# Kernel optimization log

Hardware: AMD Instinct MI355X
Metric: run time of the kernel (lower is better)

## Reference

```python
import jax, jax.numpy as jnp
import numpy as np


def setup_inputs() -> dict:
    key = jax.random.key(0)
    kq, kv, ks = jax.random.split(key, 3)
    B, T, nh, N, D = 4, 2048, 8, 64, 128
    Q = jax.random.normal(kq, (B, T, nh, N), dtype=jnp.float32)
    V = jax.random.normal(kv, (B, T, D), dtype=jnp.float32)
    state = jax.random.normal(ks, (B, nh, N, D), dtype=jnp.float32)
    return {"Q": Q, "V": V, "state": state, "return_new_state": 1}


def reference(Q, V, state, return_new_state):
    # Inter-chunk: read recurrent state.  Q:[B,T,nh,N] x state:[B,nh,N,D] -> [B,T,nh,D]
    output = jnp.einsum('BTnN,BnND->BTnD', Q, state)
    new_state = None
    if return_new_state:
        # Q.flatten(2).mT @ V, unflattened: outer-product accumulation Q^T V
        new_state = state + jnp.einsum('BTnN,BTD->BnND', Q, V)
    T = Q.shape[1]
    if T > 1:
        # Strictly-causal intra-chunk term: tril(QQ^T, -1) @ V
        scores = jnp.tril(jnp.einsum('BTnN,BUnN->BnTU', Q, Q), k=-1)
        output = output + jnp.einsum('BnTU,BUD->BTnD', scores, V)
    return (output, new_state)
```

## Files before the change

kernel.cpp:

```cpp
#include <hip/hip_runtime.h>


using floatx4 = __attribute__((ext_vector_type(4))) float;
using float4v = __attribute__((ext_vector_type(4))) float;
using float2v = __attribute__((ext_vector_type(2))) float;
using shortx8 = __attribute__((ext_vector_type(8))) short;
using shortx4 = __attribute__((ext_vector_type(4))) short;
using uint2v  = __attribute__((ext_vector_type(2))) unsigned int;

#define MFMA16(a, b, c) __builtin_amdgcn_mfma_f32_16x16x32_bf16((a), (b), (c), 0, 0, 0)

__device__ __forceinline__ unsigned short f2bf(float f) {
  unsigned int u = __builtin_bit_cast(unsigned int, f);
  u += 0x7FFFu + ((u >> 16) & 1u);
  return (unsigned short)(u >> 16);
}
__device__ __forceinline__ float bf2f(unsigned short h) {
  unsigned int u = ((unsigned int)h) << 16;
  return __builtin_bit_cast(float, u);
}
__device__ __forceinline__ unsigned int pack2(float a, float b) {
  return (unsigned int)f2bf(a) | ((unsigned int)f2bf(b) << 16);
}
__device__ __forceinline__ shortx8 lds8(const unsigned short* p) {
  shortx4 a = *(const shortx4*)p;
  shortx4 b = *(const shortx4*)(p + 4);
  return __builtin_shufflevector(a, b, 0, 1, 2, 3, 4, 5, 6, 7);
}

#define DECODE_BNC()                                    \
  const int id = blockIdx.x;                            \
  const int n = (id >> 3) & 7;                          \
  const int bc = (id >> 6) * 8 + (id & 7);              \
  const int b = bc >> 5, c = bc & 31

__global__ __launch_bounds__(256) void k_phase1(const float* __restrict__ Q,
                                                const float* __restrict__ V,
                                                unsigned short* __restrict__ ws1) {
  __shared__ unsigned short Qt[64 * 68];
  __shared__ unsigned short Vt[128 * 68];

  DECODE_BNC();
  const int tid = threadIdx.x;
  const float* qbase = Q + (((size_t)(b * 2048 + c * 64) * 8 + n) * 64);
  const float* vbase = V + ((size_t)(b * 2048 + c * 64) * 128);

#pragma unroll
  for (int it = 0; it < 8; ++it) {
    int j = tid + it * 256;
    int i = j & 63, p = j >> 6;
    float q0 = qbase[(2 * p) * 512 + i];
    float q1 = qbase[(2 * p + 1) * 512 + i];
    *(unsigned int*)&Qt[i * 68 + 2 * p] = pack2(q0, q1);
  }
#pragma unroll
  for (int it = 0; it < 16; ++it) {
    int j = tid + it * 256;
    int d = j & 127, p = j >> 7;
    float v0 = vbase[(2 * p) * 128 + d];
    float v1 = vbase[(2 * p + 1) * 128 + d];
    *(unsigned int*)&Vt[d * 68 + 2 * p] = pack2(v0, v1);
  }
  __syncthreads();

  const int wave = tid >> 6, lane = tid & 63;
  const int col = lane & 15, quad = lane >> 4;

  floatx4 acc[4][2];
#pragma unroll
  for (int ti = 0; ti < 4; ++ti)
#pragma unroll
    for (int dj = 0; dj < 2; ++dj) acc[ti][dj] = (floatx4){0.f, 0.f, 0.f, 0.f};

#pragma unroll
  for (int s = 0; s < 2; ++s) {
    const int koff = s * 32 + quad * 8;
    shortx8 bv[2];
#pragma unroll
    for (int dj = 0; dj < 2; ++dj)
      bv[dj] = lds8(&Vt[((wave * 2 + dj) * 16 + col) * 68 + koff]);
#pragma unroll
    for (int ti = 0; ti < 4; ++ti) {
      shortx8 aq = lds8(&Qt[(ti * 16 + col) * 68 + koff]);
#pragma unroll
      for (int dj = 0; dj < 2; ++dj) acc[ti][dj] = MFMA16(aq, bv[dj], acc[ti][dj]);
    }
  }

  unsigned short* wbase = ws1 + (size_t)((b * 8 + n) * 32 + c) * 8192;
#pragma unroll
  for (int ti = 0; ti < 4; ++ti)
#pragma unroll
    for (int dj = 0; dj < 2; ++dj)
#pragma unroll
      for (int r = 0; r < 4; ++r) {
        int i = ti * 16 + quad * 4 + r;
        int d = (wave * 2 + dj) * 16 + col;
        wbase[i * 128 + d] = f2bf(acc[ti][dj][r]);
      }
}

__global__ __launch_bounds__(256) void k_prefix(const float* __restrict__ state,
                                                const unsigned int* __restrict__ ws1,
                                                unsigned int* __restrict__ ws2,
                                                float* __restrict__ new_state) {
  int t = blockIdx.x * 256 + threadIdx.x;
  int bn = t >> 12;
  int e2 = t & 4095;
  float2v st = *(const float2v*)(state + (size_t)bn * 8192 + 2 * e2);
  float run0 = st.x, run1 = st.y;
  const unsigned int* w1 = ws1 + (size_t)bn * 32 * 4096 + e2;
  unsigned int* w2 = ws2 + (size_t)bn * 32 * 4096 + e2;
#pragma unroll
  for (int g = 0; g < 32; ++g) {
    w2[g * 4096] = pack2(run0, run1);
    unsigned int s = w1[g * 4096];
    run0 += bf2f((unsigned short)(s & 0xFFFFu));
    run1 += bf2f((unsigned short)(s >> 16));
  }
  float2v ns; ns.x = run0; ns.y = run1;
  *(float2v*)(new_state + (size_t)bn * 8192 + 2 * e2) = ns;
}

__global__ __launch_bounds__(256) void k_phase2(const float* __restrict__ Q,
                                                const float* __restrict__ V,
                                                const unsigned short* __restrict__ ws2,
                                                float* __restrict__ out) {
  __shared__ unsigned short Qs[64 * 72];
  __shared__ unsigned short Vt[128 * 68];
  __shared__ unsigned short Ss[64 * 72];
  __shared__ unsigned short Pt[128 * 68];

  DECODE_BNC();
  const int tid = threadIdx.x;
  const int wave = tid >> 6, lane = tid & 63;
  const int col = lane & 15, quad = lane >> 4;

  {
    const unsigned int* pb32 =
        (const unsigned int*)(ws2 + (size_t)((b * 8 + n) * 32 + c) * 8192);
#pragma unroll
    for (int it = 0; it < 16; ++it) {
      int j = tid + it * 256;
      int d2 = j & 63, i = j >> 6;
      unsigned int u = pb32[i * 64 + d2];
      Pt[(2 * d2) * 68 + i] = (unsigned short)(u & 0xFFFFu);
      Pt[(2 * d2 + 1) * 68 + i] = (unsigned short)(u >> 16);
    }
  }

  const float* qbase = Q + (((size_t)(b * 2048 + c * 64) * 8 + n) * 64);
  const float* vbase = V + ((size_t)(b * 2048 + c * 64) * 128);
  float* obase = out + (((size_t)(b * 2048 + c * 64) * 8 + n) * 128);

#pragma unroll
  for (int it = 0; it < 4; ++it) {
    int l = tid + it * 256;
    int t = l >> 4, k4 = (l & 15) * 4;
    float4v q = *(const float4v*)(qbase + (size_t)t * 512 + k4);
    uint2v u;
    u.x = pack2(q.x, q.y);
    u.y = pack2(q.z, q.w);
    *(uint2v*)&Qs[t * 72 + k4] = u;
  }
#pragma unroll
  for (int it = 0; it < 16; ++it) {
    int j = tid + it * 256;
    int d = j & 127, p = j >> 7;
    float v0 = vbase[(size_t)(2 * p) * 128 + d];
    float v1 = vbase[(size_t)(2 * p + 1) * 128 + d];
    *(unsigned int*)&Vt[d * 68 + 2 * p] = pack2(v0, v1);
  }
  __syncthreads();

  {
    int job = 0;
    for (int ti = 0; ti < 4; ++ti)
      for (int ui = 0; ui <= (ti | 1); ++ui, ++job) {
        if ((job & 3) != wave) continue;
        if (ui > ti) {
#pragma unroll
          for (int r = 0; r < 4; ++r)
            Ss[(ti * 16 + quad * 4 + r) * 72 + ui * 16 + col] = 0;
        } else {
          floatx4 sc = (floatx4){0.f, 0.f, 0.f, 0.f};
#pragma unroll
          for (int s = 0; s < 2; ++s) {
            shortx8 at = *(const shortx8*)&Qs[(ti * 16 + col) * 72 + s * 32 + quad * 8];
            shortx8 au = *(const shortx8*)&Qs[(ui * 16 + col) * 72 + s * 32 + quad * 8];
            sc = MFMA16(at, au, sc);
          }
#pragma unroll
          for (int r = 0; r < 4; ++r) {
            int t = ti * 16 + quad * 4 + r, u = ui * 16 + col;
            Ss[t * 72 + u] = (u < t) ? f2bf(sc[r]) : (unsigned short)0;
          }
        }
      }
  }
  __syncthreads();

  floatx4 acc[4][2];
#pragma unroll
  for (int ti = 0; ti < 4; ++ti)
#pragma unroll
    for (int dj = 0; dj < 2; ++dj) acc[ti][dj] = (floatx4){0.f, 0.f, 0.f, 0.f};

#pragma unroll
  for (int s = 0; s < 2; ++s) {
    const int koff = s * 32 + quad * 8;
    shortx8 bp[2];
#pragma unroll
    for (int dj = 0; dj < 2; ++dj)
      bp[dj] = lds8(&Pt[((wave * 2 + dj) * 16 + col) * 68 + koff]);
#pragma unroll
    for (int ti = 0; ti < 4; ++ti) {
      shortx8 aq = *(const shortx8*)&Qs[(ti * 16 + col) * 72 + koff];
#pragma unroll
      for (int dj = 0; dj < 2; ++dj) acc[ti][dj] = MFMA16(aq, bp[dj], acc[ti][dj]);
    }
  }
#pragma unroll
  for (int s = 0; s < 2; ++s) {
    const int koff = s * 32 + quad * 8;
    shortx8 bv[2];
#pragma unroll
    for (int dj = 0; dj < 2; ++dj)
      bv[dj] = lds8(&Vt[((wave * 2 + dj) * 16 + col) * 68 + koff]);
    for (int ti = (s == 0 ? 0 : 2); ti < 4; ++ti) {
      shortx8 as = *(const shortx8*)&Ss[(ti * 16 + col) * 72 + koff];
#pragma unroll
      for (int dj = 0; dj < 2; ++dj) acc[ti][dj] = MFMA16(as, bv[dj], acc[ti][dj]);
    }
  }
#pragma unroll
  for (int ti = 0; ti < 4; ++ti)
#pragma unroll
    for (int dj = 0; dj < 2; ++dj)
#pragma unroll
      for (int r = 0; r < 4; ++r) {
        int t = ti * 16 + quad * 4 + r;
        int d = (wave * 2 + dj) * 16 + col;
        obase[(size_t)t * 1024 + d] = acc[ti][dj][r];
      }
}

extern "C" void kernel_launch(void* const* d_in, const int* in_sizes, int n_in,
                              void* d_out, int out_size, void* d_ws, size_t ws_size,
                              hipStream_t stream) {
  (void)in_sizes; (void)n_in; (void)out_size; (void)ws_size;
  const float* Q     = (const float*)d_in[0];
  const float* V     = (const float*)d_in[1];
  const float* state = (const float*)d_in[2];
  float* out        = (float*)d_out;
  float* new_state  = out + (size_t)4 * 2048 * 8 * 128;
  unsigned short* ws1 = (unsigned short*)d_ws;
  unsigned short* ws2 = ws1 + (size_t)32 * 32 * 8192;

  k_phase1<<<1024, 256, 0, stream>>>(Q, V, ws1);
  k_prefix<<<512, 256, 0, stream>>>(state, (const unsigned int*)ws1,
                                    (unsigned int*)ws2, new_state);
  k_phase2<<<1024, 256, 0, stream>>>(Q, V, ws2, out);
}
```

Baseline: 104.6 us.

## Fuse three phases into one cooperative kernel with grid-wide syncs

Replaces the three separate launches (phase1, prefix scan, phase2) with one cooperative kernel of 512 blocks that runs each phase back to back, separated by grid.sync barriers. Each block handles two chunk jobs per phase, and the original three launches remain as a fallback if the cooperative launch fails. The goal is to remove launch gaps and inter-kernel drain. In exchange, occupancy is capped at two blocks per CU, work per block is serialized, and grid barriers add cost. The bf16 pack helper also switches to the library conversion intrinsic.

After: 345.0 us. 230% more time.

```diff
diff --git a/kernel.cpp b/kernel.cpp
--- a/kernel.cpp
+++ b/kernel.cpp
@@ -1,4 +1,8 @@
 #include <hip/hip_runtime.h>
+#include <hip/hip_bf16.h>
+#include <hip/hip_cooperative_groups.h>
+
+namespace cg = cooperative_groups;
 
 
 using floatx4 = __attribute__((ext_vector_type(4))) float;
@@ -20,7 +24,10 @@
   return __builtin_bit_cast(float, u);
 }
 __device__ __forceinline__ unsigned int pack2(float a, float b) {
-  return (unsigned int)f2bf(a) | ((unsigned int)f2bf(b) << 16);
+  __hip_bfloat162 h = __float22bfloat162_rn(float2{a, b});
+  unsigned int u;
+  __builtin_memcpy(&u, &h, 4);
+  return u;
 }
 __device__ __forceinline__ shortx8 lds8(const unsigned short* p) {
   shortx4 a = *(const shortx4*)p;
@@ -28,20 +35,20 @@
   return __builtin_shufflevector(a, b, 0, 1, 2, 3, 4, 5, 6, 7);
 }
 
-#define DECODE_BNC()                                    \
-  const int id = blockIdx.x;                            \
-  const int n = (id >> 3) & 7;                          \
-  const int bc = (id >> 6) * 8 + (id & 7);              \
+#define DECODE_JOB(job)                                 \
+  const int n = ((job) >> 3) & 7;                       \
+  const int bc = ((job) >> 6) * 8 + ((job) & 7);        \
   const int b = bc >> 5, c = bc & 31
 
-__global__ __launch_bounds__(256) void k_phase1(const float* __restrict__ Q,
-                                                const float* __restrict__ V,
-                                                unsigned short* __restrict__ ws1) {
-  __shared__ unsigned short Qt[64 * 68];
-  __shared__ unsigned short Vt[128 * 68];
-
-  DECODE_BNC();
-  const int tid = threadIdx.x;
+__device__ __forceinline__ void phase1_body(int job, int tid,
+                                            const float* __restrict__ Q,
+                                            const float* __restrict__ V,
+                                            unsigned short* __restrict__ ws1,
+                                            unsigned short* Qt,
+                                            unsigned short* Vt) {
+  DECODE_JOB(job);
+  const int wave = tid >> 6, lane = tid & 63;
+  const int col = lane & 15, quad = lane >> 4;
   const float* qbase = Q + (((size_t)(b * 2048 + c * 64) * 8 + n) * 64);
   const float* vbase = V + ((size_t)(b * 2048 + c * 64) * 128);
 
@@ -63,9 +70,6 @@
   }
   __syncthreads();
 
-  const int wave = tid >> 6, lane = tid & 63;
-  const int col = lane & 15, quad = lane >> 4;
-
   floatx4 acc[4][2];
 #pragma unroll
   for (int ti = 0; ti < 4; ++ti)
@@ -100,17 +104,17 @@
       }
 }
 
-__global__ __launch_bounds__(256) void k_prefix(const float* __restrict__ state,
-                                                const unsigned int* __restrict__ ws1,
-                                                unsigned int* __restrict__ ws2,
-                                                float* __restrict__ new_state) {
-  int t = blockIdx.x * 256 + threadIdx.x;
+__device__ __forceinline__ void prefix_body(int t,
+                                            const float* __restrict__ state,
+                                            const unsigned int* __restrict__ w1base,
+                                            unsigned int* __restrict__ w2base,
+                                            float* __restrict__ new_state) {
   int bn = t >> 12;
   int e2 = t & 4095;
   float2v st = *(const float2v*)(state + (size_t)bn * 8192 + 2 * e2);
   float run0 = st.x, run1 = st.y;
-  const unsigned int* w1 = ws1 + (size_t)bn * 32 * 4096 + e2;
-  unsigned int* w2 = ws2 + (size_t)bn * 32 * 4096 + e2;
+  const unsigned int* w1 = w1base + (size_t)bn * 131072 + e2;
+  unsigned int* w2 = w2base + (size_t)bn * 131072 + e2;
 #pragma unroll
   for (int g = 0; g < 32; ++g) {
     w2[g * 4096] = pack2(run0, run1);
@@ -122,17 +126,16 @@
   *(float2v*)(new_state + (size_t)bn * 8192 + 2 * e2) = ns;
 }
 
-__global__ __launch_bounds__(256) void k_phase2(const float* __restrict__ Q,
-                                                const float* __restrict__ V,
-                                                const unsigned short* __restrict__ ws2,
-                                                float* __restrict__ out) {
-  __shared__ unsigned short Qs[64 * 72];
-  __shared__ unsigned short Vt[128 * 68];
-  __shared__ unsigned short Ss[64 * 72];
-  __shared__ unsigned short Pt[128 * 68];
-
-  DECODE_BNC();
-  const int tid = threadIdx.x;
+__device__ __forceinline__ void phase2_body(int job, int tid,
+                                            const float* __restrict__ Q,
+                                            const float* __restrict__ V,
+                                            const unsigned short* __restrict__ ws2,
+                                            float* __restrict__ out,
+                                            unsigned short* Qs,
+                                            unsigned short* Vt,
+                                            unsigned short* Ss,
+                                            unsigned short* Pt) {
+  DECODE_JOB(job);
   const int wave = tid >> 6, lane = tid & 63;
   const int col = lane & 15, quad = lane >> 4;
 
@@ -148,7 +151,6 @@
       Pt[(2 * d2 + 1) * 68 + i] = (unsigned short)(u >> 16);
     }
   }
-
   const float* qbase = Q + (((size_t)(b * 2048 + c * 64) * 8 + n) * 64);
   const float* vbase = V + ((size_t)(b * 2048 + c * 64) * 128);
   float* obase = out + (((size_t)(b * 2048 + c * 64) * 8 + n) * 128);
@@ -174,10 +176,10 @@
   __syncthreads();
 
   {
-    int job = 0;
+    int w = 0;
     for (int ti = 0; ti < 4; ++ti)
-      for (int ui = 0; ui <= (ti | 1); ++ui, ++job) {
-        if ((job & 3) != wave) continue;
+      for (int ui = 0; ui <= (ti | 1); ++ui, ++w) {
+        if ((w & 3) != wave) continue;
         if (ui > ti) {
 #pragma unroll
           for (int r = 0; r < 4; ++r)
@@ -243,6 +245,60 @@
         int d = (wave * 2 + dj) * 16 + col;
         obase[(size_t)t * 1024 + d] = acc[ti][dj][r];
       }
+}
+
+__global__ __launch_bounds__(256, 2) void k_fused(
+    const float* __restrict__ Q, const float* __restrict__ V,
+    const float* __restrict__ state, unsigned short* __restrict__ ws1,
+    unsigned short* __restrict__ ws2, float* __restrict__ out,
+    float* __restrict__ new_state) {
+  __shared__ __align__(16) unsigned short smem[26624];
+  cg::grid_group grid = cg::this_grid();
+
+  const int bid = blockIdx.x;
+  const int tid = threadIdx.x;
+
+  phase1_body(bid, tid, Q, V, ws1, smem, smem + 4352);
+  __syncthreads();
+  phase1_body(bid + 512, tid, Q, V, ws1, smem, smem + 4352);
+
+  __threadfence();
+  grid.sync();
+
+  prefix_body(bid * 256 + tid, state, (const unsigned int*)ws1,
+              (unsigned int*)ws2, new_state);
+
+  __threadfence();
+  grid.sync();
+
+  phase2_body(bid, tid, Q, V, ws2, out,
+              smem, smem + 4608, smem + 13312, smem + 17920);
+  __syncthreads();
+  phase2_body(bid + 512, tid, Q, V, ws2, out,
+              smem, smem + 4608, smem + 13312, smem + 17920);
+}
+
+__global__ __launch_bounds__(256) void k_phase1(const float* __restrict__ Q,
+                                                const float* __restrict__ V,
+                                                unsigned short* __restrict__ ws1) {
+  __shared__ __align__(16) unsigned short smem[13056];
+  phase1_body(blockIdx.x, threadIdx.x, Q, V, ws1, smem, smem + 4352);
+}
+
+__global__ __launch_bounds__(256) void k_prefix(const float* __restrict__ state,
+                                                const unsigned int* __restrict__ ws1,
+                                                unsigned int* __restrict__ ws2,
+                                                float* __restrict__ new_state) {
+  prefix_body(blockIdx.x * 256 + threadIdx.x, state, ws1, ws2, new_state);
+}
+
+__global__ __launch_bounds__(256) void k_phase2(const float* __restrict__ Q,
+                                                const float* __restrict__ V,
+                                                const unsigned short* __restrict__ ws2,
+                                                float* __restrict__ out) {
+  __shared__ __align__(16) unsigned short smem[26624];
+  phase2_body(blockIdx.x, threadIdx.x, Q, V, ws2, out,
+              smem, smem + 4608, smem + 13312, smem + 17920);
 }
 
 extern "C" void kernel_launch(void* const* d_in, const int* in_sizes, int n_in,
@@ -257,8 +313,14 @@
   unsigned short* ws1 = (unsigned short*)d_ws;
   unsigned short* ws2 = ws1 + (size_t)32 * 32 * 8192;
 
-  k_phase1<<<1024, 256, 0, stream>>>(Q, V, ws1);
-  k_prefix<<<512, 256, 0, stream>>>(state, (const unsigned int*)ws1,
-                                    (unsigned int*)ws2, new_state);
-  k_phase2<<<1024, 256, 0, stream>>>(Q, V, ws2, out);
-}
+  void* args[] = {(void*)&Q, (void*)&V, (void*)&state, (void*)&ws1,
+                  (void*)&ws2, (void*)&out, (void*)&new_state};
+  hipError_t err = hipLaunchCooperativeKernel((void*)k_fused, dim3(512), dim3(256),
+                                              args, 0, stream);
+  if (err != hipSuccess) {
+    k_phase1<<<1024, 256, 0, stream>>>(Q, V, ws1);
+    k_prefix<<<512, 256, 0, stream>>>(state, (const unsigned int*)ws1,
+                                      (unsigned int*)ws2, new_state);
+    k_phase2<<<1024, 256, 0, stream>>>(Q, V, ws2, out);
+  }
+}
```

## Store workspace in MFMA-fragment order and stage output through LDS for coalesced writes

Applied to the files above, without the earlier changes.

Phase 1 now writes its per-chunk Q^T V partials in the MFMA accumulator fragment order as packed 16-byte vectors instead of scattered 2-byte stores. The prefix kernel and phase 2 decode that permuted layout, and phase 2 places the pairs into a transposed LDS tile with 4-byte stores. Phase 2 also stages its output tile in shared memory and writes it back as coalesced float4 rows. These changes target uncoalesced global stores, at the cost of an extra LDS round trip with two barriers and strided state and new_state accesses in the prefix kernel. Packing now uses the HIP bf16 intrinsic.

Measured after the change: 103.5 us. About the same (-1.0%).

```diff
diff --git a/kernel.cpp b/kernel.cpp
--- a/kernel.cpp
+++ b/kernel.cpp
@@ -1,12 +1,13 @@
 #include <hip/hip_runtime.h>
+#include <hip/hip_bf16.h>
 
 
 using floatx4 = __attribute__((ext_vector_type(4))) float;
 using float4v = __attribute__((ext_vector_type(4))) float;
-using float2v = __attribute__((ext_vector_type(2))) float;
 using shortx8 = __attribute__((ext_vector_type(8))) short;
 using shortx4 = __attribute__((ext_vector_type(4))) short;
 using uint2v  = __attribute__((ext_vector_type(2))) unsigned int;
+using uint4v  = __attribute__((ext_vector_type(4))) unsigned int;
 
 #define MFMA16(a, b, c) __builtin_amdgcn_mfma_f32_16x16x32_bf16((a), (b), (c), 0, 0, 0)
 
@@ -20,7 +21,10 @@
   return __builtin_bit_cast(float, u);
 }
 __device__ __forceinline__ unsigned int pack2(float a, float b) {
-  return (unsigned int)f2bf(a) | ((unsigned int)f2bf(b) << 16);
+  __hip_bfloat162 h = __float22bfloat162_rn(float2{a, b});
+  unsigned int u;
+  __builtin_memcpy(&u, &h, 4);
+  return u;
 }
 __device__ __forceinline__ shortx8 lds8(const unsigned short* p) {
   shortx4 a = *(const shortx4*)p;
@@ -28,20 +32,21 @@
   return __builtin_shufflevector(a, b, 0, 1, 2, 3, 4, 5, 6, 7);
 }
 
-#define DECODE_BNC()                                    \
-  const int id = blockIdx.x;                            \
-  const int n = (id >> 3) & 7;                          \
-  const int bc = (id >> 6) * 8 + (id & 7);              \
+#define DECODE_JOB(job)                                 \
+  const int n = ((job) >> 3) & 7;                       \
+  const int bc = ((job) >> 6) * 8 + ((job) & 7);        \
   const int b = bc >> 5, c = bc & 31
 
 __global__ __launch_bounds__(256) void k_phase1(const float* __restrict__ Q,
                                                 const float* __restrict__ V,
-                                                unsigned short* __restrict__ ws1) {
-  __shared__ unsigned short Qt[64 * 68];
-  __shared__ unsigned short Vt[128 * 68];
-
-  DECODE_BNC();
+                                                unsigned int* __restrict__ ws1) {
+  __shared__ __align__(16) unsigned short Qt[64 * 68];
+  __shared__ __align__(16) unsigned short Vt[128 * 68];
+
+  DECODE_JOB(blockIdx.x);
   const int tid = threadIdx.x;
+  const int wave = tid >> 6, lane = tid & 63;
+  const int col = lane & 15, quad = lane >> 4;
   const float* qbase = Q + (((size_t)(b * 2048 + c * 64) * 8 + n) * 64);
   const float* vbase = V + ((size_t)(b * 2048 + c * 64) * 128);
 
@@ -63,9 +68,6 @@
   }
   __syncthreads();
 
-  const int wave = tid >> 6, lane = tid & 63;
-  const int col = lane & 15, quad = lane >> 4;
-
   floatx4 acc[4][2];
 #pragma unroll
   for (int ti = 0; ti < 4; ++ti)
@@ -87,17 +89,16 @@
     }
   }
 
-  unsigned short* wbase = ws1 + (size_t)((b * 8 + n) * 32 + c) * 8192;
-#pragma unroll
-  for (int ti = 0; ti < 4; ++ti)
-#pragma unroll
-    for (int dj = 0; dj < 2; ++dj)
-#pragma unroll
-      for (int r = 0; r < 4; ++r) {
-        int i = ti * 16 + quad * 4 + r;
-        int d = (wave * 2 + dj) * 16 + col;
-        wbase[i * 128 + d] = f2bf(acc[ti][dj][r]);
-      }
+  unsigned int* wbase = ws1 + (size_t)((b * 8 + n) * 32 + c) * 4096;
+#pragma unroll
+  for (int k = 0; k < 4; ++k) {
+    uint4v X;
+    X.x = pack2(acc[k][0][0], acc[k][0][1]);
+    X.y = pack2(acc[k][0][2], acc[k][0][3]);
+    X.z = pack2(acc[k][1][0], acc[k][1][1]);
+    X.w = pack2(acc[k][1][2], acc[k][1][3]);
+    *(uint4v*)(wbase + k * 1024 + tid * 4) = X;
+  }
 }
 
 __global__ __launch_bounds__(256) void k_prefix(const float* __restrict__ state,
@@ -106,11 +107,15 @@
                                                 float* __restrict__ new_state) {
   int t = blockIdx.x * 256 + threadIdx.x;
   int bn = t >> 12;
-  int e2 = t & 4095;
-  float2v st = *(const float2v*)(state + (size_t)bn * 8192 + 2 * e2);
-  float run0 = st.x, run1 = st.y;
-  const unsigned int* w1 = ws1 + (size_t)bn * 32 * 4096 + e2;
-  unsigned int* w2 = ws2 + (size_t)bn * 32 * 4096 + e2;
+  int p = t & 4095;
+  int k = p >> 10, tid0 = (p >> 2) & 255, e = p & 3;
+  int i0 = k * 16 + ((tid0 >> 4) & 3) * 4 + (e & 1) * 2;
+  int d  = ((tid0 >> 6) * 2 + (e >> 1)) * 16 + (tid0 & 15);
+  const float* sbase = state + (size_t)bn * 8192;
+  float run0 = sbase[i0 * 128 + d];
+  float run1 = sbase[(i0 + 1) * 128 + d];
+  const unsigned int* w1 = ws1 + (size_t)bn * 131072 + p;
+  unsigned int* w2 = ws2 + (size_t)bn * 131072 + p;
 #pragma unroll
   for (int g = 0; g < 32; ++g) {
     w2[g * 4096] = pack2(run0, run1);
@@ -118,37 +123,38 @@
     run0 += bf2f((unsigned short)(s & 0xFFFFu));
     run1 += bf2f((unsigned short)(s >> 16));
   }
-  float2v ns; ns.x = run0; ns.y = run1;
-  *(float2v*)(new_state + (size_t)bn * 8192 + 2 * e2) = ns;
+  float* nbase = new_state + (size_t)bn * 8192;
+  nbase[i0 * 128 + d] = run0;
+  nbase[(i0 + 1) * 128 + d] = run1;
 }
 
 __global__ __launch_bounds__(256) void k_phase2(const float* __restrict__ Q,
                                                 const float* __restrict__ V,
-                                                const unsigned short* __restrict__ ws2,
+                                                const unsigned int* __restrict__ ws2,
                                                 float* __restrict__ out) {
-  __shared__ unsigned short Qs[64 * 72];
-  __shared__ unsigned short Vt[128 * 68];
-  __shared__ unsigned short Ss[64 * 72];
-  __shared__ unsigned short Pt[128 * 68];
-
-  DECODE_BNC();
+  __shared__ __align__(16) unsigned short smem[27136];
+  unsigned short* Qs = smem;
+  unsigned short* Vt = smem + 4608;
+  unsigned short* Ss = smem + 13312;
+  unsigned short* Pt = smem + 17920;
+
+  DECODE_JOB(blockIdx.x);
   const int tid = threadIdx.x;
   const int wave = tid >> 6, lane = tid & 63;
   const int col = lane & 15, quad = lane >> 4;
 
   {
-    const unsigned int* pb32 =
-        (const unsigned int*)(ws2 + (size_t)((b * 8 + n) * 32 + c) * 8192);
+    const unsigned int* pb32 = ws2 + (size_t)((b * 8 + n) * 32 + c) * 4096;
 #pragma unroll
     for (int it = 0; it < 16; ++it) {
       int j = tid + it * 256;
-      int d2 = j & 63, i = j >> 6;
-      unsigned int u = pb32[i * 64 + d2];
-      Pt[(2 * d2) * 68 + i] = (unsigned short)(u & 0xFFFFu);
-      Pt[(2 * d2 + 1) * 68 + i] = (unsigned short)(u >> 16);
-    }
-  }
-
+      int k = j >> 10, tid0 = (j >> 2) & 255, e = j & 3;
+      int i0 = k * 16 + ((tid0 >> 4) & 3) * 4 + (e & 1) * 2;
+      int d  = ((tid0 >> 6) * 2 + (e >> 1)) * 16 + (tid0 & 15);
+      unsigned int u = pb32[j];
+      *(unsigned int*)&Pt[d * 72 + i0] = u;
+    }
+  }
   const float* qbase = Q + (((size_t)(b * 2048 + c * 64) * 8 + n) * 64);
   const float* vbase = V + ((size_t)(b * 2048 + c * 64) * 128);
   float* obase = out + (((size_t)(b * 2048 + c * 64) * 8 + n) * 128);
@@ -174,10 +180,10 @@
   __syncthreads();
 
   {
-    int job = 0;
+    int w = 0;
     for (int ti = 0; ti < 4; ++ti)
-      for (int ui = 0; ui <= (ti | 1); ++ui, ++job) {
-        if ((job & 3) != wave) continue;
+      for (int ui = 0; ui <= (ti | 1); ++ui, ++w) {
+        if ((w & 3) != wave) continue;
         if (ui > ti) {
 #pragma unroll
           for (int r = 0; r < 4; ++r)
@@ -212,7 +218,7 @@
     shortx8 bp[2];
 #pragma unroll
     for (int dj = 0; dj < 2; ++dj)
-      bp[dj] = lds8(&Pt[((wave * 2 + dj) * 16 + col) * 68 + koff]);
+      bp[dj] = *(const shortx8*)&Pt[((wave * 2 + dj) * 16 + col) * 72 + koff];
 #pragma unroll
     for (int ti = 0; ti < 4; ++ti) {
       shortx8 aq = *(const shortx8*)&Qs[(ti * 16 + col) * 72 + koff];
@@ -233,6 +239,9 @@
       for (int dj = 0; dj < 2; ++dj) acc[ti][dj] = MFMA16(as, bv[dj], acc[ti][dj]);
     }
   }
+
+  __syncthreads();
+  float* Ob = (float*)smem;
 #pragma unroll
   for (int ti = 0; ti < 4; ++ti)
 #pragma unroll
@@ -241,8 +250,16 @@
       for (int r = 0; r < 4; ++r) {
         int t = ti * 16 + quad * 4 + r;
         int d = (wave * 2 + dj) * 16 + col;
-        obase[(size_t)t * 1024 + d] = acc[ti][dj][r];
+        Ob[t * 132 + d] = acc[ti][dj][r];
       }
+  __syncthreads();
+#pragma unroll
+  for (int it = 0; it < 8; ++it) {
+    int j = tid + it * 256;
+    int t = j >> 5, dq = j & 31;
+    float4v o = *(const float4v*)&Ob[t * 132 + dq * 4];
+    *(float4v*)(obase + (size_t)t * 1024 + dq * 4) = o;
+  }
 }
 
 extern "C" void kernel_launch(void* const* d_in, const int* in_sizes, int n_in,
@@ -254,11 +271,10 @@
   const float* state = (const float*)d_in[2];
   float* out        = (float*)d_out;
   float* new_state  = out + (size_t)4 * 2048 * 8 * 128;
-  unsigned short* ws1 = (unsigned short*)d_ws;
-  unsigned short* ws2 = ws1 + (size_t)32 * 32 * 8192;
+  unsigned int* ws1 = (unsigned int*)d_ws;
+  unsigned int* ws2 = ws1 + (size_t)32 * 131072;
 
   k_phase1<<<1024, 256, 0, stream>>>(Q, V, ws1);
-  k_prefix<<<512, 256, 0, stream>>>(state, (const unsigned int*)ws1,
-                                    (unsigned int*)ws2, new_state);
+  k_prefix<<<512, 256, 0, stream>>>(state, ws1, ws2, new_state);
   k_phase2<<<1024, 256, 0, stream>>>(Q, V, ws2, out);
 }
```
